# Kernel optimization log

Measured on AMD Instinct MI355X. Metric: run time of the kernel, lower is better.

The kernel has to match this reference:

```python
import jax, jax.numpy as jnp
import numpy as np
from jax import lax

DN = ('NCDHW', 'OIDHW', 'NCDHW')  # dimension numbers matching torch Conv3d (cross-correlation)


def setup_inputs() -> dict:
    key = jax.random.key(0)
    k0, k1, k2, k3 = jax.random.split(key, 4)
    B, P, C = 32, 2048, 512
    x = jax.random.normal(k0, (B, P, C), dtype=jnp.float32)
    w1 = jax.random.normal(k1, (1, 1, 1, 1, 1), dtype=jnp.float32)
    w2 = jax.random.normal(k2, (1, 1, 2, 2, 2), dtype=jnp.float32)
    w3 = jax.random.normal(k3, (1, 1, 3, 3, 3), dtype=jnp.float32)
    return {"x": x, "w1": w1, "w2": w2, "w3": w3}


def reference(x, w1, w2, w3):
    B, P, C = x.shape
    t = P // 16
    # [B,P,C] -> [B,C,t,4,4]
    xv = jnp.transpose(x, (0, 2, 1)).reshape(B, C, t, 4, 4)
    # x_shift: [B,t,C,4,4] -> [B*t, C, 4, 4]
    x_shift = jnp.transpose(xv, (0, 2, 1, 3, 4)).reshape(B * t, C, 4, 4)
    # channel mean -> [B,1,t,4,4]
    xm = jnp.mean(xv, axis=1, keepdims=True)
    # ST_1: 1x1x1 conv, no pad
    p1 = lax.conv_general_dilated(xm, w1, (1, 1, 1), 'VALID', dimension_numbers=DN)
    # ST_2: pad (left=1 on t,h,w), then 2x2x2 valid conv -> same shape
    xp = jnp.pad(xm, ((0, 0), (0, 0), (1, 0), (1, 0), (1, 0)))
    p2 = lax.conv_general_dilated(xp, w2, (1, 1, 1), 'VALID', dimension_numbers=DN)
    # ST_3: 3x3x3 conv with padding 1 -> same shape
    p3 = lax.conv_general_dilated(xm, w3, (1, 1, 1), [(1, 1), (1, 1), (1, 1)], dimension_numbers=DN)
    g = p1 + p2 + p3  # [B,1,t,4,4]
    # transpose(2,1) -> [B,t,1,4,4] -> [B*t,1,4,4]
    g = jnp.transpose(g, (0, 2, 1, 3, 4)).reshape(B * t, 1, 4, 4)
    out = x_shift * jax.nn.sigmoid(g)  # broadcast over C
    # back to [B,P,C]
    out = out.reshape(B, t, C, 4, 4)
    out = jnp.transpose(out, (0, 2, 1, 3, 4)).reshape(B, C, P)
    return jnp.transpose(out, (0, 2, 1))
```

## Files before the change

### kernel.cpp

```cpp
#include <hip/hip_runtime.h>
#include <math.h>

#define BB 32
#define PP 2048
#define CC 512
#define TT 128
#define NROWS (BB*PP)

__global__ __launch_bounds__(256) void fused_kernel(
        const float* __restrict__ x,
        const float* __restrict__ w1, const float* __restrict__ w2,
        const float* __restrict__ w3, float* __restrict__ out) {
    __shared__ float smean[3][16];
    __shared__ float spart[4][8];
    __shared__ float sgate[16];

    int bid = blockIdx.x;
    int wg  = ((bid & 7) << 9) | (bid >> 3);
    int b = wg >> 7;
    int t = wg & 127;

    int tid  = threadIdx.x;
    int wave = tid >> 6;
    int lane = tid & 63;

    size_t tile_f4 = ((size_t)(b * TT + t) * 16) * (CC / 4);
    const float4* xt = (const float4*)x + tile_f4;
    float4*       ot = (float4*)out     + tile_f4;

    float4 v[8];
    #pragma unroll
    for (int j = 0; j < 8; ++j) v[j] = xt[tid + 256 * j];

    int hr    = tid >> 3;
    int hu    = tid & 7;
    int plane = hr >> 4;
    int rloc  = hr & 15;
    int ht    = t + (plane ? 1 : -1);
    bool hvalid = (ht >= 0) && (ht < TT);
    float hsum = 0.0f;
    if (hvalid) {
        const float4* hrow = (const float4*)x +
            ((size_t)(b * TT + ht) * 16 + rloc) * (CC / 4);
        #pragma unroll
        for (int j = 0; j < 16; ++j) {
            float4 hv = hrow[hu + 8 * j];
            hsum += (hv.x + hv.y) + (hv.z + hv.w);
        }
    }

    if (tid < 48) ((float*)smean)[tid] = 0.0f;

    #pragma unroll
    for (int j = 0; j < 8; ++j) {
        float s = (v[j].x + v[j].y) + (v[j].z + v[j].w);
        #pragma unroll
        for (int off = 32; off > 0; off >>= 1)
            s += __shfl_down(s, off, 64);
        if (lane == 0) spart[wave][j] = s;
    }

    hsum += __shfl_down(hsum, 4, 64);
    hsum += __shfl_down(hsum, 2, 64);
    hsum += __shfl_down(hsum, 1, 64);

    __syncthreads();

    if (hu == 0 && hvalid)
        smean[plane ? 2 : 0][rloc] = hsum * (1.0f / 512.0f);
    if (tid < 16) {
        int jj = tid >> 1;
        float s = (tid & 1) ? (spart[2][jj] + spart[3][jj])
                            : (spart[0][jj] + spart[1][jj]);
        smean[1][tid] = s * (1.0f / 512.0f);
    }

    __syncthreads();

    if (tid < 16) {
        int h  = tid >> 2;
        int w_ = tid & 3;
        float g = 0.0f;
        #pragma unroll
        for (int i = 0; i < 3; ++i) {
            #pragma unroll
            for (int j = 0; j < 3; ++j) {
                int hh = h + j - 1;
                if (hh < 0 || hh > 3) continue;
                #pragma unroll
                for (int k = 0; k < 3; ++k) {
                    int ww = w_ + k - 1;
                    if (ww < 0 || ww > 3) continue;
                    float wt = w3[i * 9 + j * 3 + k];
                    if (i < 2 && j < 2 && k < 2) wt += w2[i * 4 + j * 2 + k];
                    if (i == 1 && j == 1 && k == 1) wt += w1[0];
                    g += wt * smean[i][hh * 4 + ww];
                }
            }
        }
        sgate[tid] = 1.0f / (1.0f + __expf(-g));
    }

    __syncthreads();

    #pragma unroll
    for (int j = 0; j < 8; ++j) {
        float s = sgate[(tid + 256 * j) >> 7];
        float4 o = v[j];
        o.x *= s; o.y *= s; o.z *= s; o.w *= s;
        ot[tid + 256 * j] = o;
    }
}

extern "C" void kernel_launch(void* const* d_in, const int* in_sizes, int n_in,
                              void* d_out, int out_size, void* d_ws, size_t ws_size,
                              hipStream_t stream) {
    const float* x  = (const float*)d_in[0];
    const float* w1 = (const float*)d_in[1];
    const float* w2 = (const float*)d_in[2];
    const float* w3 = (const float*)d_in[3];
    float* out = (float*)d_out;

    fused_kernel<<<BB * TT, 256, 0, stream>>>(x, w1, w2, w3, out);
}
```

Baseline: 243.3 us.

## Split fused kernel into separate mean and gate-scale kernels

Replaces the single fused kernel, which re-read the neighbouring time tiles to recompute their channel means, with two kernels. The first writes per-tile channel means to workspace, and the second reads the three neighbouring mean planes, computes the gate and scales x. This removes the halo re-read of adjacent tiles, about twice the tile size, but reads x twice across two launches and drops the XCD-aware block remapping. The second read of x (128 MB) may partly hit in the large last-level cache.

```diff
diff --git a/kernel.cpp b/kernel.cpp
--- a/kernel.cpp
+++ b/kernel.cpp
@@ -6,75 +6,58 @@
 #define CC 512
 #define TT 128
 #define NROWS (BB*PP)
+#define NTILES (BB*TT)
 
-__global__ __launch_bounds__(256) void fused_kernel(
-        const float* __restrict__ x,
-        const float* __restrict__ w1, const float* __restrict__ w2,
-        const float* __restrict__ w3, float* __restrict__ out) {
-    __shared__ float smean[3][16];
+__global__ __launch_bounds__(256) void mean_kernel(
+        const float* __restrict__ x, float* __restrict__ mean) {
     __shared__ float spart[4][8];
-    __shared__ float sgate[16];
-
-    int bid = blockIdx.x;
-    int wg  = ((bid & 7) << 9) | (bid >> 3);
-    int b = wg >> 7;
-    int t = wg & 127;
-
+    int bid  = blockIdx.x;
     int tid  = threadIdx.x;
     int wave = tid >> 6;
     int lane = tid & 63;
 
-    size_t tile_f4 = ((size_t)(b * TT + t) * 16) * (CC / 4);
-    const float4* xt = (const float4*)x + tile_f4;
-    float4*       ot = (float4*)out     + tile_f4;
-
-    float4 v[8];
-    #pragma unroll
-    for (int j = 0; j < 8; ++j) v[j] = xt[tid + 256 * j];
-
-    int hr    = tid >> 3;
-    int hu    = tid & 7;
-    int plane = hr >> 4;
-    int rloc  = hr & 15;
-    int ht    = t + (plane ? 1 : -1);
-    bool hvalid = (ht >= 0) && (ht < TT);
-    float hsum = 0.0f;
-    if (hvalid) {
-        const float4* hrow = (const float4*)x +
-            ((size_t)(b * TT + ht) * 16 + rloc) * (CC / 4);
-        #pragma unroll
-        for (int j = 0; j < 16; ++j) {
-            float4 hv = hrow[hu + 8 * j];
-            hsum += (hv.x + hv.y) + (hv.z + hv.w);
-        }
-    }
-
-    if (tid < 48) ((float*)smean)[tid] = 0.0f;
-
+    const float4* xt = (const float4*)x + (size_t)bid * 2048;
+    float p[8];
     #pragma unroll
     for (int j = 0; j < 8; ++j) {
-        float s = (v[j].x + v[j].y) + (v[j].z + v[j].w);
+        float4 v = xt[tid + 256 * j];
+        p[j] = (v.x + v.y) + (v.z + v.w);
+    }
+    #pragma unroll
+    for (int j = 0; j < 8; ++j) {
+        float s = p[j];
         #pragma unroll
         for (int off = 32; off > 0; off >>= 1)
             s += __shfl_down(s, off, 64);
         if (lane == 0) spart[wave][j] = s;
     }
-
-    hsum += __shfl_down(hsum, 4, 64);
-    hsum += __shfl_down(hsum, 2, 64);
-    hsum += __shfl_down(hsum, 1, 64);
-
     __syncthreads();
-
-    if (hu == 0 && hvalid)
-        smean[plane ? 2 : 0][rloc] = hsum * (1.0f / 512.0f);
     if (tid < 16) {
         int jj = tid >> 1;
         float s = (tid & 1) ? (spart[2][jj] + spart[3][jj])
                             : (spart[0][jj] + spart[1][jj]);
-        smean[1][tid] = s * (1.0f / 512.0f);
+        mean[bid * 16 + tid] = s * (1.0f / 512.0f);
     }
+}
 
+__global__ __launch_bounds__(256) void gate_scale_kernel(
+        const float* __restrict__ x, const float* __restrict__ mean,
+        const float* __restrict__ w1, const float* __restrict__ w2,
+        const float* __restrict__ w3, float* __restrict__ out) {
+    __shared__ float sm[3][16];
+    __shared__ float sgate[16];
+    int bid = blockIdx.x;
+    int b = bid >> 7;
+    int t = bid & 127;
+    int tid = threadIdx.x;
+
+    if (tid < 48) {
+        int plane = tid >> 4;
+        int r     = tid & 15;
+        int tv    = t + plane - 1;
+        sm[plane][r] = (tv >= 0 && tv < TT)
+                         ? mean[(b * TT + tv) * 16 + r] : 0.0f;
+    }
     __syncthreads();
 
     if (tid < 16) {
@@ -94,21 +77,23 @@
                     float wt = w3[i * 9 + j * 3 + k];
                     if (i < 2 && j < 2 && k < 2) wt += w2[i * 4 + j * 2 + k];
                     if (i == 1 && j == 1 && k == 1) wt += w1[0];
-                    g += wt * smean[i][hh * 4 + ww];
+                    g += wt * sm[i][hh * 4 + ww];
                 }
             }
         }
         sgate[tid] = 1.0f / (1.0f + __expf(-g));
     }
-
     __syncthreads();
 
+    const float4* xt = (const float4*)x + (size_t)bid * 2048;
+    float4*       ot = (float4*)out     + (size_t)bid * 2048;
     #pragma unroll
     for (int j = 0; j < 8; ++j) {
-        float s = sgate[(tid + 256 * j) >> 7];
-        float4 o = v[j];
-        o.x *= s; o.y *= s; o.z *= s; o.w *= s;
-        ot[tid + 256 * j] = o;
+        int idx = tid + 256 * j;
+        float s = sgate[idx >> 7];
+        float4 v = xt[idx];
+        v.x *= s; v.y *= s; v.z *= s; v.w *= s;
+        ot[idx] = v;
     }
 }
 
@@ -119,7 +104,9 @@
     const float* w1 = (const float*)d_in[1];
     const float* w2 = (const float*)d_in[2];
     const float* w3 = (const float*)d_in[3];
-    float* out = (float*)d_out;
+    float* out  = (float*)d_out;
+    float* mean = (float*)d_ws;
 
-    fused_kernel<<<BB * TT, 256, 0, stream>>>(x, w1, w2, w3, out);
+    mean_kernel<<<NTILES, 256, 0, stream>>>(x, mean);
+    gate_scale_kernel<<<NTILES, 256, 0, stream>>>(x, mean, w1, w2, w3, out);
 }
```

After: 254.7 us. 4.7% more time.
